# Kernel tuning notes

Hardware: AMD Instinct MI355X
Metric: run time of the kernel (lower is better)

The kernel has to match this reference:

```python
import jax, jax.numpy as jnp
import numpy as np

TAGSET = 5
START = 3  # tag_to_ix['<START>']
STOP = 4   # tag_to_ix['<STOP>']
NEG_INF = -10000.0


def setup_inputs() -> dict:
    key = jax.random.key(0)
    ks = jax.random.split(key, 12)
    T, V, E, H = 4096, 50000, 1024, 512  # seq_len, vocab, embed_dim, per-direction hidden
    scale = 0.02
    sentence = jax.random.randint(ks[0], (T,), 0, V)
    embed = jax.random.normal(ks[1], (V, E), jnp.float32) * scale
    W_ih_f = jax.random.normal(ks[2], (4 * H, E), jnp.float32) * scale
    W_hh_f = jax.random.normal(ks[3], (4 * H, H), jnp.float32) * scale
    b_f = jnp.zeros((4 * H,), jnp.float32)
    W_ih_b = jax.random.normal(ks[4], (4 * H, E), jnp.float32) * scale
    W_hh_b = jax.random.normal(ks[5], (4 * H, H), jnp.float32) * scale
    b_b = jnp.zeros((4 * H,), jnp.float32)
    h0 = jax.random.normal(ks[6], (2, H), jnp.float32) * scale
    c0 = jax.random.normal(ks[7], (2, H), jnp.float32) * scale
    W_out = jax.random.normal(ks[8], (TAGSET, 2 * H), jnp.float32) * scale
    b_out = jnp.zeros((TAGSET,), jnp.float32)
    transitions = jax.random.normal(ks[9], (TAGSET, TAGSET), jnp.float32)
    transitions = transitions.at[START, :].set(NEG_INF).at[:, STOP].set(NEG_INF)
    return dict(sentence=sentence, embed=embed, W_ih_f=W_ih_f, W_hh_f=W_hh_f, b_f=b_f,
                W_ih_b=W_ih_b, W_hh_b=W_hh_b, b_b=b_b, h0=h0, c0=c0,
                W_out=W_out, b_out=b_out, transitions=transitions)


def _lstm_dir(x, W_ih, W_hh, b, h0, c0):
    # x: [T, E]; single-layer LSTM, PyTorch gate order i,f,g,o
    def step(carry, xt):
        h, c = carry
        gates = W_ih @ xt + W_hh @ h + b  # [4H]
        i, f, g, o = jnp.split(gates, 4)
        i = jax.nn.sigmoid(i)
        f = jax.nn.sigmoid(f)
        g = jnp.tanh(g)
        o = jax.nn.sigmoid(o)
        c = f * c + i * g
        h = o * jnp.tanh(c)
        return (h, c), h
    _, hs = jax.lax.scan(step, (h0, c0), x)
    return hs  # [T, H]


def reference(sentence, embed, W_ih_f, W_hh_f, b_f, W_ih_b, W_hh_b, b_b, h0, c0, W_out, b_out, transitions):
    # BiLSTM features
    x = embed[sentence]                       # [T, E]
    hf = _lstm_dir(x, W_ih_f, W_hh_f, b_f, h0[0], c0[0])
    hb = _lstm_dir(x[::-1], W_ih_b, W_hh_b, b_b, h0[1], c0[1])[::-1]
    feats = jnp.concatenate([hf, hb], axis=-1) @ W_out.T + b_out  # [T, 5]

    # Viterbi decode
    init = jnp.full((TAGSET,), NEG_INF, feats.dtype).at[START].set(0.0)

    def vstep(fv, feat):
        scores = fv[None, :] + transitions    # [next_tag, prev_tag]
        bp = jnp.argmax(scores, axis=1)       # backpointers
        fv_new = jnp.max(scores, axis=1) + feat
        return fv_new, bp

    fv, bptrs = jax.lax.scan(vstep, init, feats)  # bptrs: [T, 5]
    terminal = fv + transitions[STOP]
    best_last = jnp.argmax(terminal)
    score = jnp.max(terminal)

    # Backtrack: original uses rows T-1 .. 1 of the backpointer table
    def back(y, bp):
        prev = bp[y]
        return prev, prev
    _, rev = jax.lax.scan(back, best_last, bptrs[1:][::-1])
    path = jnp.concatenate([rev[::-1], best_last[None]])  # [T], tag ids in order
    return score, path
```

## Files before the change

### kernel.cpp

```cpp
#include <hip/hip_runtime.h>
#include <hip/hip_bf16.h>


#define T_LEN 4096
#define EDIM  1024
#define HID   512
#define G4    2048

typedef short short8 __attribute__((ext_vector_type(8)));
typedef float f32x4  __attribute__((ext_vector_type(4)));

__device__ __forceinline__ float bf16_to_f32(unsigned bits) {
  return __uint_as_float(bits << 16);
}
__device__ __forceinline__ unsigned bf16rne(float f) {
  unsigned u = __float_as_uint(f);
  return (u + 0x7fffu + ((u >> 16) & 1u)) >> 16;
}

__global__ __launch_bounds__(256) void gather_kernel(
    const int* __restrict__ sent, const float* __restrict__ embed,
    unsigned short* __restrict__ xbf)
{
  const int t = blockIdx.x;
  const int tok = sent[t];
  const int e = threadIdx.x * 4;
  const float4 v = *(const float4*)(embed + (size_t)tok * EDIM + e);
  uint2 o;
  o.x = bf16rne(v.x) | (bf16rne(v.y) << 16);
  o.y = bf16rne(v.z) | (bf16rne(v.w) << 16);
  *(uint2*)(xbf + (size_t)t * EDIM + e) = o;
}

__global__ __launch_bounds__(256) void convw_kernel(
    const float* __restrict__ Wf, const float* __restrict__ Wb,
    unsigned short* __restrict__ of, unsigned short* __restrict__ ob)
{
  const float* src = blockIdx.z ? Wb : Wf;
  unsigned short* dst = blockIdx.z ? ob : of;
  const size_t idx = (size_t)blockIdx.x * 2048 + (size_t)threadIdx.x * 8;
  const float4 a = *(const float4*)(src + idx);
  const float4 b = *(const float4*)(src + idx + 4);
  uint4 o;
  o.x = bf16rne(a.x) | (bf16rne(a.y) << 16);
  o.y = bf16rne(a.z) | (bf16rne(a.w) << 16);
  o.z = bf16rne(b.x) | (bf16rne(b.y) << 16);
  o.w = bf16rne(b.z) | (bf16rne(b.w) << 16);
  *(uint4*)(dst + idx) = o;
}

__global__ __launch_bounds__(512) void inith_kernel(
    const float* __restrict__ h0, unsigned* __restrict__ hcF,
    unsigned* __restrict__ hcB)
{
  unsigned* hc = blockIdx.x ? hcB : hcF;
  const int j = threadIdx.x;
  hc[j] = bf16rne(h0[blockIdx.x * HID + j]);
}

__global__ __launch_bounds__(256) void gemm_x_kernel(
    const unsigned short* __restrict__ xbf,
    const unsigned short* __restrict__ Wfb, const unsigned short* __restrict__ Wbb,
    const float* __restrict__ biasF, const float* __restrict__ biasB,
    float* __restrict__ Xf, float* __restrict__ Xb)
{
  const int zz = blockIdx.z;
  const unsigned short* Bp = zz ? Wbb : Wfb;
  const float* bias = zz ? biasB : biasF;
  float* C = zz ? Xb : Xf;
  const int n0 = blockIdx.x * 64;
  const int m0 = blockIdx.y * 64;
  __shared__ unsigned short As[64][40];
  __shared__ unsigned short Bs[64][40];
  const int tid = threadIdx.x;
  const int wv = tid >> 6, lane = tid & 63;
  const int moff = (wv >> 1) * 32, noff = (wv & 1) * 32;
  const int lrow = tid >> 2, lseg = (tid & 3) * 8;
  const int fr = lane & 15;
  const int fk = (lane >> 4) * 8;
  f32x4 acc[2][2];
#pragma unroll
  for (int i = 0; i < 2; i++)
#pragma unroll
    for (int j = 0; j < 2; j++) acc[i][j] = (f32x4){0.f, 0.f, 0.f, 0.f};

  for (int k0 = 0; k0 < EDIM; k0 += 32) {
    const uint4 av = *(const uint4*)(xbf + (size_t)(m0 + lrow) * EDIM + k0 + lseg);
    const uint4 bv = *(const uint4*)(Bp  + (size_t)(n0 + lrow) * EDIM + k0 + lseg);
    *(uint4*)&As[lrow][lseg] = av;
    *(uint4*)&Bs[lrow][lseg] = bv;
    __syncthreads();
    short8 af[2], bg[2];
#pragma unroll
    for (int i = 0; i < 2; i++) af[i] = *(const short8*)&As[moff + i * 16 + fr][fk];
#pragma unroll
    for (int j = 0; j < 2; j++) bg[j] = *(const short8*)&Bs[noff + j * 16 + fr][fk];
#pragma unroll
    for (int i = 0; i < 2; i++)
#pragma unroll
      for (int j = 0; j < 2; j++)
        acc[i][j] = __builtin_amdgcn_mfma_f32_16x16x32_bf16(af[i], bg[j], acc[i][j], 0, 0, 0);
    __syncthreads();
  }
#pragma unroll
  for (int i = 0; i < 2; i++)
#pragma unroll
    for (int j = 0; j < 2; j++) {
      const int col = n0 + noff + j * 16 + fr;
      const float bv = bias[col];
#pragma unroll
      for (int r = 0; r < 4; r++) {
        const int row = m0 + moff + i * 16 + (lane >> 4) * 4 + r;
        C[(size_t)row * G4 + col] = acc[i][j][r] + bv;
      }
    }
}

__global__ __launch_bounds__(512) void lstm_kernel(
    const float* __restrict__ WhhF, const float* __restrict__ WhhB,
    const float* __restrict__ Xf, const float* __restrict__ Xb,
    const float* __restrict__ c0,
    unsigned* __restrict__ hcF, unsigned* __restrict__ hcB)
{
  const int wg = blockIdx.x;
  const int dir = wg >> 5;
  const int w = wg & 31;
  const float* Whh = dir ? WhhB : WhhF;
  const float* X   = dir ? Xb : Xf;
  unsigned* hcomm  = dir ? hcB : hcF;

  const int tid = threadIdx.x;
  const int g = tid >> 5;
  const int c = tid & 31;

  __shared__ float hl[HID];
  __shared__ float gl[64];
  __shared__ float xl[64];
  __shared__ float cl[16];

  float wreg[4][16];
#pragma unroll
  for (int rr = 0; rr < 4; ++rr) {
    const int r = g * 4 + rr;
    const int grow = (r >> 4) * HID + w * 16 + (r & 15);
#pragma unroll
    for (int kk = 0; kk < 16; ++kk)
      wreg[rr][kk] = Whh[(size_t)grow * HID + c * 16 + kk];
  }
  if (tid < 16) cl[tid] = c0[dir * HID + w * 16 + tid];
  __syncthreads();

  for (int s = 0; s < T_LEN; ++s) {
    float xv = 0.f;
    const int xrow = dir ? (T_LEN - 1 - s) : s;
    if (tid < 64)
      xv = X[(size_t)xrow * G4 + (tid >> 4) * HID + w * 16 + (tid & 15)];

    unsigned v;
    const unsigned want = (unsigned)s;
    for (;;) {
      v = __hip_atomic_load(&hcomm[(size_t)s * HID + tid],
                            __ATOMIC_RELAXED, __HIP_MEMORY_SCOPE_AGENT);
      if (__syncthreads_count((int)((v >> 16) == want)) == 512) break;
      __builtin_amdgcn_s_sleep(1);
    }
    hl[tid] = bf16_to_f32(v & 0xffffu);
    __syncthreads();

    float p0 = 0.f, p1 = 0.f, p2 = 0.f, p3 = 0.f;
    const float4* hp = (const float4*)&hl[c * 16];
    float4 h4[4];
    h4[0] = hp[0]; h4[1] = hp[1]; h4[2] = hp[2]; h4[3] = hp[3];
    const float* hh = (const float*)h4;
#pragma unroll
    for (int kk = 0; kk < 16; ++kk) {
      const float hv = hh[kk];
      p0 += wreg[0][kk] * hv;
      p1 += wreg[1][kk] * hv;
      p2 += wreg[2][kk] * hv;
      p3 += wreg[3][kk] * hv;
    }
#pragma unroll
    for (int m = 1; m < 32; m <<= 1) {
      p0 += __shfl_xor(p0, m, 64);
      p1 += __shfl_xor(p1, m, 64);
      p2 += __shfl_xor(p2, m, 64);
      p3 += __shfl_xor(p3, m, 64);
    }
    if (c == 0) gl[g * 4 + 0] = p0;
    if (c == 1) gl[g * 4 + 1] = p1;
    if (c == 2) gl[g * 4 + 2] = p2;
    if (c == 3) gl[g * 4 + 3] = p3;
    if (tid < 64) xl[tid] = xv;
    __syncthreads();

    if (tid < 16) {
      const int jj = tid;
      const float gi = gl[jj]      + xl[jj];
      const float gf = gl[16 + jj] + xl[16 + jj];
      const float gg = gl[32 + jj] + xl[32 + jj];
      const float go = gl[48 + jj] + xl[48 + jj];
      const float ii = 1.f / (1.f + expf(-gi));
      const float ff = 1.f / (1.f + expf(-gf));
      const float tg = tanhf(gg);
      const float oo = 1.f / (1.f + expf(-go));
      const float cn = ff * cl[jj] + ii * tg;
      cl[jj] = cn;
      const float h = oo * tanhf(cn);
      const unsigned pk = ((unsigned)(s + 1) << 16) | bf16rne(h);
      __hip_atomic_store(&hcomm[(size_t)(s + 1) * HID + w * 16 + jj], pk,
                         __ATOMIC_RELAXED, __HIP_MEMORY_SCOPE_AGENT);
    }
  }
}

__global__ __launch_bounds__(320) void feats_kernel(
    const unsigned* __restrict__ hcF, const unsigned* __restrict__ hcB,
    const float* __restrict__ Wout, const float* __restrict__ bout,
    float* __restrict__ feats)
{
  const int t = blockIdx.x;
  const int tag = threadIdx.x >> 6;
  const int lane = threadIdx.x & 63;
  const unsigned* hf = hcF + (size_t)(t + 1) * HID;
  const unsigned* hb = hcB + (size_t)(T_LEN - t) * HID;
  float sum = 0.f;
  for (int e = lane; e < HID; e += 64) {
    sum += Wout[tag * 1024 + e]       * bf16_to_f32(hf[e] & 0xffffu);
    sum += Wout[tag * 1024 + 512 + e] * bf16_to_f32(hb[e] & 0xffffu);
  }
#pragma unroll
  for (int m = 1; m < 64; m <<= 1) sum += __shfl_xor(sum, m, 64);
  if (lane == 0) feats[t * 5 + tag] = sum + bout[tag];
}

__device__ __forceinline__ unsigned map_compose(unsigned a, unsigned b) {
  unsigned r = 0;
#pragma unroll
  for (int i = 0; i < 5; ++i) {
    const unsigned gi = (b >> (3 * i)) & 7u;
    r |= ((a >> (3 * gi)) & 7u) << (3 * i);
  }
  return r;
}

__global__ __launch_bounds__(64) void viterbi_kernel(
    const float* __restrict__ feats, const float* __restrict__ trans,
    float* __restrict__ out)
{
  __shared__ float fe[2][2560];
  __shared__ unsigned char bpb[5][T_LEN];
  const int lane = threadIdx.x;
  const int n = lane >> 3, p = lane & 7;
  const bool act = (n < 5) && (p < 5);
  const int nn = (n < 5) ? n : 0;
  const float tr = act ? trans[n * 5 + p] : -3.0e38f;
  float fvp = (p == 3) ? 0.f : -10000.f;

  for (int i = lane; i < 2560; i += 64) fe[0][i] = feats[i];
  __syncthreads();

  for (int ch = 0; ch < 8; ++ch) {
    const int buf = ch & 1;
    float pf[40];
    if (ch < 7) {
#pragma unroll
      for (int i = 0; i < 40; ++i)
        pf[i] = feats[(ch + 1) * 2560 + i * 64 + lane];
    }
    for (int tt = 0; tt < 512; ++tt) {
      const int t = ch * 512 + tt;
      float s = act ? (fvp + tr) : -3.0e38f;
      float bm = s; int bp_ = p;
#pragma unroll
      for (int d = 1; d < 8; d <<= 1) {
        const float os = __shfl_xor(bm, d, 64);
        const int   op = __shfl_xor(bp_, d, 64);
        if (os > bm || (os == bm && op < bp_)) { bm = os; bp_ = op; }
      }
      const float fvn = bm + fe[buf][tt * 5 + nn];
      if (p == 0 && n < 5) bpb[n][t] = (unsigned char)bp_;
      fvp = __shfl(fvn, p * 8, 64);
    }
    __syncthreads();
    if (ch < 7) {
#pragma unroll
      for (int i = 0; i < 40; ++i) fe[buf ^ 1][i * 64 + lane] = pf[i];
    }
    __syncthreads();
  }

  float tv = (lane < 5) ? (fvp + trans[4 * 5 + lane]) : -3.0e38f;
  int bl = lane;
#pragma unroll
  for (int d = 1; d < 8; d <<= 1) {
    const float ov = __shfl_xor(tv, d, 64);
    const int   ol = __shfl_xor(bl, d, 64);
    if (ov > tv || (ov == tv && ol < bl)) { tv = ov; bl = ol; }
  }
  const float score = __shfl(tv, 0, 64);
  const int best = __shfl(bl, 0, 64);
  if (lane == 0) out[0] = score;

  const unsigned IDENT = 0u | (1u << 3) | (2u << 6) | (3u << 9) | (4u << 12);
  const int lo = lane * 64;
  unsigned msave[64];
  unsigned comp = IDENT;
#pragma unroll
  for (int tt = 0; tt < 64; ++tt) {
    const int t = lo + tt;
    unsigned mt;
    if (t == 0) mt = IDENT;
    else
      mt = (unsigned)bpb[0][t] | ((unsigned)bpb[1][t] << 3) |
           ((unsigned)bpb[2][t] << 6) | ((unsigned)bpb[3][t] << 9) |
           ((unsigned)bpb[4][t] << 12);
    msave[tt] = mt;
    comp = map_compose(comp, mt);
  }
  unsigned inc = comp;
#pragma unroll
  for (int d = 1; d < 64; d <<= 1) {
    const unsigned other = __shfl_down(inc, d, 64);
    const unsigned comb = map_compose(inc, other);
    if (lane + d < 64) inc = comb;
  }
  unsigned exc = __shfl_down(inc, 1, 64);
  if (lane == 63) exc = IDENT;

  int y = (int)((exc >> (3 * best)) & 7u);
  out[1 + lo + 63] = (float)y;
#pragma unroll
  for (int tt = 63; tt >= 0; --tt) {
    const int t = lo + tt;
    if (t == 0) break;
    y = (int)((msave[tt] >> (3 * y)) & 7u);
    out[1 + t - 1] = (float)y;
  }
}

extern "C" void kernel_launch(void* const* d_in, const int* in_sizes, int n_in,
                              void* d_out, int out_size, void* d_ws, size_t ws_size,
                              hipStream_t stream) {
  const int*   sent   = (const int*)d_in[0];
  const float* embed  = (const float*)d_in[1];
  const float* W_ih_f = (const float*)d_in[2];
  const float* W_hh_f = (const float*)d_in[3];
  const float* b_f    = (const float*)d_in[4];
  const float* W_ih_b = (const float*)d_in[5];
  const float* W_hh_b = (const float*)d_in[6];
  const float* b_b    = (const float*)d_in[7];
  const float* h0     = (const float*)d_in[8];
  const float* c0     = (const float*)d_in[9];
  const float* W_out  = (const float*)d_in[10];
  const float* b_out  = (const float*)d_in[11];
  const float* trans  = (const float*)d_in[12];

  char* ws = (char*)d_ws;
  float*          Xf    = (float*)(ws + 0);
  float*          Xb    = (float*)(ws + 33554432);
  unsigned short* xbf   = (unsigned short*)(ws + 67108864);
  unsigned short* Wfb   = (unsigned short*)(ws + 75497472);
  unsigned short* Wbb   = (unsigned short*)(ws + 79691776);
  unsigned*       hcF   = (unsigned*)(ws + 83886080);
  unsigned*       hcB   = (unsigned*)(ws + 92276736);
  float*          feats = (float*)(ws + 100667392);
  float*          out   = (float*)d_out;

  gather_kernel<<<T_LEN, 256, 0, stream>>>(sent, embed, xbf);
  convw_kernel<<<dim3(1024, 1, 2), 256, 0, stream>>>(W_ih_f, W_ih_b, Wfb, Wbb);
  inith_kernel<<<2, 512, 0, stream>>>(h0, hcF, hcB);
  gemm_x_kernel<<<dim3(32, 64, 2), 256, 0, stream>>>(xbf, Wfb, Wbb, b_f, b_b, Xf, Xb);
  lstm_kernel<<<64, 512, 0, stream>>>(W_hh_f, W_hh_b, Xf, Xb, c0, hcF, hcB);
  feats_kernel<<<T_LEN, 320, 0, stream>>>(hcF, hcB, W_out, b_out, feats);
  viterbi_kernel<<<1, 64, 0, stream>>>(feats, trans, out);
}
```

Before: 11.70 ms.

## Restructure LSTM recurrence to one hidden unit per wave with wave-local sync

The persistent LSTM kernel now runs 256 blocks of 4 waves, with each wave owning one hidden unit across all four gates. Each wave polls the whole previous h vector using 64-bit atomic loads and checks readiness with a wave-level vote, so no block-wide barriers or shared memory are needed on each step. The dot product is reduced with DPP row operations, and the gate nonlinearities use fast exp2/rcp approximations. This spreads the recurrence over more CUs and cuts intra-block barrier latency on the serial critical path, at the cost of more global polling traffic and lower-precision activation math.

```diff
diff --git a/kernel.cpp b/kernel.cpp
--- a/kernel.cpp
+++ b/kernel.cpp
@@ -16,6 +16,24 @@
 __device__ __forceinline__ unsigned bf16rne(float f) {
   unsigned u = __float_as_uint(f);
   return (u + 0x7fffu + ((u >> 16) & 1u)) >> 16;
+}
+
+__device__ __forceinline__ float wave_sum64(float x) {
+  int t;
+  t = __builtin_amdgcn_update_dpp(0, __float_as_int(x), 0x111, 0xf, 0xf, true); x += __int_as_float(t);
+  t = __builtin_amdgcn_update_dpp(0, __float_as_int(x), 0x112, 0xf, 0xf, true); x += __int_as_float(t);
+  t = __builtin_amdgcn_update_dpp(0, __float_as_int(x), 0x114, 0xf, 0xf, true); x += __int_as_float(t);
+  t = __builtin_amdgcn_update_dpp(0, __float_as_int(x), 0x118, 0xf, 0xf, true); x += __int_as_float(t);
+  t = __builtin_amdgcn_update_dpp(0, __float_as_int(x), 0x142, 0xf, 0xf, true); x += __int_as_float(t);
+  t = __builtin_amdgcn_update_dpp(0, __float_as_int(x), 0x143, 0xf, 0xf, true); x += __int_as_float(t);
+  return x;
+}
+
+__device__ __forceinline__ float fsig(float x) {
+  return __builtin_amdgcn_rcpf(1.f + __builtin_amdgcn_exp2f(-1.44269504f * x));
+}
+__device__ __forceinline__ float ftanh(float x) {
+  return 1.f - 2.f * __builtin_amdgcn_rcpf(1.f + __builtin_amdgcn_exp2f(2.88539008f * x));
 }
 
 __global__ __launch_bounds__(256) void gather_kernel(
@@ -116,99 +134,86 @@
     }
 }
 
-__global__ __launch_bounds__(512) void lstm_kernel(
+__global__ __launch_bounds__(256) void lstm_kernel(
     const float* __restrict__ WhhF, const float* __restrict__ WhhB,
     const float* __restrict__ Xf, const float* __restrict__ Xb,
     const float* __restrict__ c0,
     unsigned* __restrict__ hcF, unsigned* __restrict__ hcB)
 {
-  const int wg = blockIdx.x;
-  const int dir = wg >> 5;
-  const int w = wg & 31;
+  const int b = blockIdx.x;
+  const int dir = b >> 7;
   const float* Whh = dir ? WhhB : WhhF;
   const float* X   = dir ? Xb : Xf;
   unsigned* hcomm  = dir ? hcB : hcF;
 
   const int tid = threadIdx.x;
-  const int g = tid >> 5;
-  const int c = tid & 31;
-
-  __shared__ float hl[HID];
-  __shared__ float gl[64];
-  __shared__ float xl[64];
-  __shared__ float cl[16];
-
-  float wreg[4][16];
-#pragma unroll
-  for (int rr = 0; rr < 4; ++rr) {
-    const int r = g * 4 + rr;
-    const int grow = (r >> 4) * HID + w * 16 + (r & 15);
-#pragma unroll
-    for (int kk = 0; kk < 16; ++kk)
-      wreg[rr][kk] = Whh[(size_t)grow * HID + c * 16 + kk];
-  }
-  if (tid < 16) cl[tid] = c0[dir * HID + w * 16 + tid];
-  __syncthreads();
+  const int g = tid >> 6;
+  const int c = tid & 63;
+  const int j = (b & 127) * 4 + g;
+
+  float wv[4][4][2];
+#pragma unroll
+  for (int gate = 0; gate < 4; ++gate) {
+    const size_t rowoff = (size_t)(gate * HID + j) * HID;
+#pragma unroll
+    for (int kk = 0; kk < 4; ++kk) {
+      const float2 w2 = *(const float2*)&Whh[rowoff + 2 * (kk * 64 + c)];
+      wv[gate][kk][0] = w2.x;
+      wv[gate][kk][1] = w2.y;
+    }
+  }
+  float cst = (c == 63) ? c0[dir * HID + j] : 0.f;
 
   for (int s = 0; s < T_LEN; ++s) {
-    float xv = 0.f;
-    const int xrow = dir ? (T_LEN - 1 - s) : s;
-    if (tid < 64)
-      xv = X[(size_t)xrow * G4 + (tid >> 4) * HID + w * 16 + (tid & 15)];
-
-    unsigned v;
+    float xg0 = 0.f, xg1 = 0.f, xg2 = 0.f, xg3 = 0.f;
+    if (c == 63) {
+      const int xrow = dir ? (T_LEN - 1 - s) : s;
+      const float* xp = X + (size_t)xrow * G4 + j;
+      xg0 = xp[0]; xg1 = xp[512]; xg2 = xp[1024]; xg3 = xp[1536];
+    }
+
     const unsigned want = (unsigned)s;
+    const unsigned long long* src =
+        (const unsigned long long*)(hcomm + (size_t)s * HID);
+    unsigned long long pv0, pv1, pv2, pv3;
     for (;;) {
-      v = __hip_atomic_load(&hcomm[(size_t)s * HID + tid],
-                            __ATOMIC_RELAXED, __HIP_MEMORY_SCOPE_AGENT);
-      if (__syncthreads_count((int)((v >> 16) == want)) == 512) break;
+      pv0 = __hip_atomic_load(&src[0 * 64 + c], __ATOMIC_RELAXED, __HIP_MEMORY_SCOPE_AGENT);
+      pv1 = __hip_atomic_load(&src[1 * 64 + c], __ATOMIC_RELAXED, __HIP_MEMORY_SCOPE_AGENT);
+      pv2 = __hip_atomic_load(&src[2 * 64 + c], __ATOMIC_RELAXED, __HIP_MEMORY_SCOPE_AGENT);
+      pv3 = __hip_atomic_load(&src[3 * 64 + c], __ATOMIC_RELAXED, __HIP_MEMORY_SCOPE_AGENT);
+      bool ok = (((pv0 >> 16) & 0xffffull) == want) & ((pv0 >> 48) == want) &
+                (((pv1 >> 16) & 0xffffull) == want) & ((pv1 >> 48) == want) &
+                (((pv2 >> 16) & 0xffffull) == want) & ((pv2 >> 48) == want) &
+                (((pv3 >> 16) & 0xffffull) == want) & ((pv3 >> 48) == want);
+      if (__all(ok)) break;
       __builtin_amdgcn_s_sleep(1);
     }
-    hl[tid] = bf16_to_f32(v & 0xffffu);
-    __syncthreads();
-
-    float p0 = 0.f, p1 = 0.f, p2 = 0.f, p3 = 0.f;
-    const float4* hp = (const float4*)&hl[c * 16];
-    float4 h4[4];
-    h4[0] = hp[0]; h4[1] = hp[1]; h4[2] = hp[2]; h4[3] = hp[3];
-    const float* hh = (const float*)h4;
-#pragma unroll
-    for (int kk = 0; kk < 16; ++kk) {
-      const float hv = hh[kk];
-      p0 += wreg[0][kk] * hv;
-      p1 += wreg[1][kk] * hv;
-      p2 += wreg[2][kk] * hv;
-      p3 += wreg[3][kk] * hv;
-    }
-#pragma unroll
-    for (int m = 1; m < 32; m <<= 1) {
-      p0 += __shfl_xor(p0, m, 64);
-      p1 += __shfl_xor(p1, m, 64);
-      p2 += __shfl_xor(p2, m, 64);
-      p3 += __shfl_xor(p3, m, 64);
-    }
-    if (c == 0) gl[g * 4 + 0] = p0;
-    if (c == 1) gl[g * 4 + 1] = p1;
-    if (c == 2) gl[g * 4 + 2] = p2;
-    if (c == 3) gl[g * 4 + 3] = p3;
-    if (tid < 64) xl[tid] = xv;
-    __syncthreads();
-
-    if (tid < 16) {
-      const int jj = tid;
-      const float gi = gl[jj]      + xl[jj];
-      const float gf = gl[16 + jj] + xl[16 + jj];
-      const float gg = gl[32 + jj] + xl[32 + jj];
-      const float go = gl[48 + jj] + xl[48 + jj];
-      const float ii = 1.f / (1.f + expf(-gi));
-      const float ff = 1.f / (1.f + expf(-gf));
-      const float tg = tanhf(gg);
-      const float oo = 1.f / (1.f + expf(-go));
-      const float cn = ff * cl[jj] + ii * tg;
-      cl[jj] = cn;
-      const float h = oo * tanhf(cn);
+
+    float a0 = 0.f, a1 = 0.f, a2 = 0.f, a3 = 0.f;
+    unsigned long long pv[4] = {pv0, pv1, pv2, pv3};
+#pragma unroll
+    for (int kk = 0; kk < 4; ++kk) {
+      const float h0 = bf16_to_f32((unsigned)pv[kk] & 0xffffu);
+      const float h1 = bf16_to_f32((unsigned)(pv[kk] >> 32) & 0xffffu);
+      a0 += wv[0][kk][0] * h0 + wv[0][kk][1] * h1;
+      a1 += wv[1][kk][0] * h0 + wv[1][kk][1] * h1;
+      a2 += wv[2][kk][0] * h0 + wv[2][kk][1] * h1;
+      a3 += wv[3][kk][0] * h0 + wv[3][kk][1] * h1;
+    }
+    a0 = wave_sum64(a0);
+    a1 = wave_sum64(a1);
+    a2 = wave_sum64(a2);
+    a3 = wave_sum64(a3);
+
+    if (c == 63) {
+      const float ii = fsig(a0 + xg0);
+      const float ff = fsig(a1 + xg1);
+      const float tg = ftanh(a2 + xg2);
+      const float oo = fsig(a3 + xg3);
+      cst = ff * cst + ii * tg;
+      const float h = oo * ftanh(cst);
       const unsigned pk = ((unsigned)(s + 1) << 16) | bf16rne(h);
-      __hip_atomic_store(&hcomm[(size_t)(s + 1) * HID + w * 16 + jj], pk,
+      __hip_atomic_store(&hcomm[(size_t)(s + 1) * HID + j], pk,
                          __ATOMIC_RELAXED, __HIP_MEMORY_SCOPE_AGENT);
     }
   }
@@ -371,7 +376,7 @@
   convw_kernel<<<dim3(1024, 1, 2), 256, 0, stream>>>(W_ih_f, W_ih_b, Wfb, Wbb);
   inith_kernel<<<2, 512, 0, stream>>>(h0, hcF, hcB);
   gemm_x_kernel<<<dim3(32, 64, 2), 256, 0, stream>>>(xbf, Wfb, Wbb, b_f, b_b, Xf, Xb);
-  lstm_kernel<<<64, 512, 0, stream>>>(W_hh_f, W_hh_b, Xf, Xb, c0, hcF, hcB);
+  lstm_kernel<<<256, 256, 0, stream>>>(W_hh_f, W_hh_b, Xf, Xb, c0, hcF, hcB);
   feats_kernel<<<T_LEN, 320, 0, stream>>>(hcF, hcB, W_out, b_out, feats);
   viterbi_kernel<<<1, 64, 0, stream>>>(feats, trans, out);
 }
```

New measurement: 19.32 ms. 1.65x slower.
